# Kernel optimization log

Hardware: AMD Instinct MI355X
Metric: run time of the kernel (lower is better)

## Reference

```python
import jax, jax.numpy as jnp
import numpy as np

DIM = 512
HEADS = 8
DIM_HEAD = 64
INNER = HEADS * DIM_HEAD
CHUNK = 32
EPS = 1e-5


def _peg_conv(x, w, b):
    # x: (B, N, C); depthwise conv1d k=3 pad=1 applied on chunks of 32
    B, N, C = x.shape
    ns = -(-N // CHUNK)
    xp = jnp.pad(x, ((0, 0), (0, ns * CHUNK - N), (0, 0)))
    xp = xp.reshape(B * ns, CHUNK, C).transpose(0, 2, 1)  # (B*ns, C, 32)
    y = jax.lax.conv_general_dilated(
        xp, w, window_strides=(1,), padding=((1, 1),),
        dimension_numbers=("NCH", "OIH", "NCH"), feature_group_count=C)
    y = y + b[None, :, None]
    y = y.transpose(0, 2, 1).reshape(B, ns * CHUNK, C)[:, :N, :]
    return y


def _peg1d(x, w, b):
    p1 = _peg_conv(x, w, b)
    sx = jnp.roll(x, CHUNK // 2, axis=1)
    p2 = jnp.roll(_peg_conv(sx, w, b), -(CHUNK // 2), axis=1)
    return x + p1 + p2


def setup_inputs() -> dict:
    key = jax.random.key(0)
    ks = jax.random.split(key, 8)
    B, N, M = 2, 4096, 1024
    x = jax.random.normal(ks[0], (B, N, DIM), dtype=jnp.float32)
    mem = jax.random.normal(ks[1], (B, M, DIM), dtype=jnp.float32)
    w_qkv = jax.random.normal(ks[2], (DIM, 3 * INNER), dtype=jnp.float32) * 0.02
    w_out = jax.random.normal(ks[3], (INNER, DIM), dtype=jnp.float32) * 0.02
    b_out = jnp.zeros((DIM,), dtype=jnp.float32)
    ln_g = jnp.ones((DIM,), dtype=jnp.float32)
    ln_b = jnp.zeros((DIM,), dtype=jnp.float32)
    pk_w = jax.random.normal(ks[4], (DIM, 1, 3), dtype=jnp.float32) * 0.1
    pk_b = jnp.zeros((DIM,), dtype=jnp.float32)
    pv_w = jax.random.normal(ks[5], (DIM, 1, 3), dtype=jnp.float32) * 0.1
    pv_b = jnp.zeros((DIM,), dtype=jnp.float32)
    return {"x": x, "mem": mem, "ln_g": ln_g, "ln_b": ln_b,
            "w_qkv": w_qkv, "w_out": w_out, "b_out": b_out,
            "pk_w": pk_w, "pk_b": pk_b, "pv_w": pv_w, "pv_b": pv_b}


def reference(x, mem, ln_g, ln_b, w_qkv, w_out, b_out, pk_w, pk_b, pv_w, pv_b):
    B, N, _ = x.shape
    # LayerNorm
    mu = jnp.mean(x, axis=-1, keepdims=True)
    var = jnp.mean(jnp.square(x - mu), axis=-1, keepdims=True)
    xn = (x - mu) * jax.lax.rsqrt(var + EPS) * ln_g + ln_b
    qkv = xn @ w_qkv  # (B, N, 3*INNER)
    q, k, v = jnp.split(qkv, 3, axis=-1)
    # memory concat
    k = jnp.concatenate((k, mem), axis=1)
    v = jnp.concatenate((v, mem), axis=1)
    # PEG1D positional conv on k,v (excluding cls token at position 0)
    k = jnp.concatenate((k[:, :1, :], _peg1d(k[:, 1:, :], pk_w, pk_b)), axis=1)
    v = jnp.concatenate((v[:, :1, :], _peg1d(v[:, 1:, :], pv_w, pv_b)), axis=1)
    # split heads: b n (h d) -> b h n d
    Nk = k.shape[1]
    qh = q.reshape(B, N, HEADS, DIM_HEAD).transpose(0, 2, 1, 3)
    kh = k.reshape(B, Nk, HEADS, DIM_HEAD).transpose(0, 2, 1, 3)
    vh = v.reshape(B, Nk, HEADS, DIM_HEAD).transpose(0, 2, 1, 3)
    scale = DIM_HEAD ** -0.5
    dots = jnp.einsum("bhnd,bhmd->bhnm", qh, kh) * scale
    attn = jax.nn.softmax(dots, axis=-1)
    out = jnp.einsum("bhnm,bhmd->bhnd", attn, vh)
    out = out.transpose(0, 2, 1, 3).reshape(B, N, INNER)
    return out @ w_out + b_out
```

## Files before the change

kernel.cpp:

```cpp
#include <hip/hip_runtime.h>
#include <hip/hip_bf16.h>

typedef short short8 __attribute__((ext_vector_type(8)));
typedef __bf16 bf16x8 __attribute__((ext_vector_type(8)));
typedef float f32x4 __attribute__((ext_vector_type(4)));
typedef float f32x8 __attribute__((ext_vector_type(8)));
typedef float f32x16 __attribute__((ext_vector_type(16)));
typedef unsigned int uint4v __attribute__((ext_vector_type(4)));

#define SEQ_N 4096
#define NKEYS 5120
#define PEG_L 5119
#define NSPLIT 2
#define KEYS_PER_SPLIT 2560
#define NT_SPLIT 40

__device__ __forceinline__ float b2f(unsigned short s){
  union{unsigned u; float f;} v; v.u = ((unsigned)s)<<16; return v.f;
}
__device__ __forceinline__ unsigned short f2b(float f){
  unsigned u = __builtin_bit_cast(unsigned, f);
  u += 0x7fffu + ((u>>16)&1u);
  return (unsigned short)(u>>16);
}
__device__ __forceinline__ unsigned cvtpk(float lo, float hi){
  unsigned r;
  asm("v_cvt_pk_bf16_f32 %0, %1, %2" : "=v"(r) : "v"(lo), "v"(hi));
  return r;
}

__global__ void k_transpose_w(const float* __restrict__ src, unsigned short* __restrict__ dst,
                              int K, int Ncols){
  __shared__ float t[32][33];
  int tx = threadIdx.x, ty = threadIdx.y;
  int bx = blockIdx.x, by = blockIdx.y;
  #pragma unroll
  for (int i=0;i<4;i++){
    int r = by*32 + ty + 8*i, c = bx*32 + tx;
    t[ty+8*i][tx] = src[(size_t)r*Ncols + c];
  }
  __syncthreads();
  #pragma unroll
  for (int i=0;i<4;i++){
    int r = bx*32 + ty + 8*i, c = by*32 + tx;
    dst[(size_t)r*K + c] = f2b(t[tx][ty+8*i]);
  }
}

__global__ __launch_bounds__(256) void k_layernorm(const float* __restrict__ x,
    const float* __restrict__ g, const float* __restrict__ bb,
    unsigned short* __restrict__ xn){
  int w = threadIdx.x >> 6, l = threadIdx.x & 63;
  int row = blockIdx.x*4 + w;
  const float* xr = x + (size_t)row*512 + l*8;
  f32x4 a = *(const f32x4*)xr;
  f32x4 c4 = *(const f32x4*)(xr+4);
  float s = a[0]+a[1]+a[2]+a[3]+c4[0]+c4[1]+c4[2]+c4[3];
  #pragma unroll
  for (int d=1; d<64; d<<=1) s += __shfl_xor(s, d);
  float mu = s * (1.0f/512.0f);
  float vs = 0.f;
  #pragma unroll
  for (int i=0;i<4;i++){ float d0=a[i]-mu; vs += d0*d0; }
  #pragma unroll
  for (int i=0;i<4;i++){ float d0=c4[i]-mu; vs += d0*d0; }
  #pragma unroll
  for (int d=1; d<64; d<<=1) vs += __shfl_xor(vs, d);
  float rstd = rsqrtf(vs*(1.0f/512.0f) + 1e-5f);
  const float* gp = g + l*8;
  const float* bp = bb + l*8;
  unsigned short o[8];
  #pragma unroll
  for (int i=0;i<8;i++){
    float xi = (i<4)? a[i] : c4[i-4];
    o[i] = f2b((xi-mu)*rstd*gp[i] + bp[i]);
  }
  *(short8*)(xn + (size_t)row*512 + l*8) = *(short8*)o;
}

__global__ void k_memcat(const float* __restrict__ mem,
                         unsigned short* __restrict__ kf, unsigned short* __restrict__ vf){
  size_t e0 = ((size_t)blockIdx.x*256 + threadIdx.x)*8;
  f32x4 a = *(const f32x4*)(mem+e0);
  f32x4 c4 = *(const f32x4*)(mem+e0+4);
  unsigned short o[8];
  #pragma unroll
  for (int i=0;i<8;i++) o[i] = f2b((i<4)? a[i] : c4[i-4]);
  int c = (int)(e0 & 511);
  size_t row = e0 >> 9;
  size_t b = row >> 10, r = row & 1023;
  size_t dst = ((b*NKEYS) + 4096 + r)*512 + c;
  *(short8*)(kf+dst) = *(short8*)o;
  *(short8*)(vf+dst) = *(short8*)o;
}

template<int EPI>
__global__ __launch_bounds__(256) void k_gemm(const unsigned short* __restrict__ A,
    const unsigned short* __restrict__ BT, const float* __restrict__ bias,
    unsigned short* __restrict__ qb, unsigned short* __restrict__ kf,
    unsigned short* __restrict__ vf, float* __restrict__ outf){
  __shared__ unsigned short Al[64][72];
  __shared__ unsigned short Bl[64][72];
  const int tid = threadIdx.x;
  const int w = tid>>6, l = tid&63, m = l&15, hh = l>>4;
  const int m0 = blockIdx.x*64, n0 = blockIdx.y*64;
  const int srow = tid>>2, scg = tid&3;
  f32x4 acc[4];
  #pragma unroll
  for (int nt=0; nt<4; ++nt) acc[nt] = f32x4{0.f,0.f,0.f,0.f};
  const unsigned short* Ap = A + (size_t)(m0+srow)*512 + scg*8;
  const unsigned short* Bp = BT + (size_t)(n0+srow)*512 + scg*8;
  for (int kt=0; kt<8; ++kt){
    short8 a0 = *(const short8*)(Ap + kt*64);
    short8 a1 = *(const short8*)(Ap + kt*64 + 32);
    short8 b0 = *(const short8*)(Bp + kt*64);
    short8 b1 = *(const short8*)(Bp + kt*64 + 32);
    __syncthreads();
    *(short8*)&Al[srow][scg*8]      = a0;
    *(short8*)&Al[srow][32+scg*8]   = a1;
    *(short8*)&Bl[srow][scg*8]      = b0;
    *(short8*)&Bl[srow][32+scg*8]   = b1;
    __syncthreads();
    #pragma unroll
    for (int ks=0; ks<2; ++ks){
      bf16x8 af = *(const bf16x8*)&Al[w*16+m][ks*32 + hh*8];
      #pragma unroll
      for (int nt=0; nt<4; ++nt){
        bf16x8 bfv = *(const bf16x8*)&Bl[nt*16+m][ks*32 + hh*8];
        acc[nt] = __builtin_amdgcn_mfma_f32_16x16x32_bf16(af, bfv, acc[nt], 0,0,0);
      }
    }
  }
  #pragma unroll
  for (int nt=0; nt<4; ++nt){
    #pragma unroll
    for (int j=0; j<4; ++j){
      int grow = m0 + w*16 + 4*hh + j;
      int gcol = n0 + nt*16 + m;
      float v = acc[nt][j];
      if (EPI==0){
        int b = grow >> 12, n = grow & 4095;
        if (gcol < 512)       qb[(size_t)grow*512 + gcol] = f2b(v);
        else if (gcol < 1024) kf[((size_t)b*NKEYS + n)*512 + (gcol-512)]  = f2b(v);
        else                  vf[((size_t)b*NKEYS + n)*512 + (gcol-1024)] = f2b(v);
      } else {
        outf[(size_t)grow*512 + gcol] = v + bias[gcol];
      }
    }
  }
}

__global__ __launch_bounds__(256) void k_peg(const unsigned short* __restrict__ in,
    const float* __restrict__ w3, const float* __restrict__ bias,
    unsigned short* __restrict__ out){
  int idx = blockIdx.x*256 + threadIdx.x;
  int cg = idx & 63;
  int i  = (idx >> 6) % NKEYS;
  int b  = (idx >> 6) / NKEYS;
  int c0 = cg*8;
  const unsigned short* base = in + (size_t)b*NKEYS*512 + c0;
  unsigned short* op = out + ((size_t)b*NKEYS + i)*512 + c0;
  if (i == 0){ *(short8*)op = *(const short8*)base; return; }
  int j = i - 1;
  float wv0[8], wv1[8], wv2[8], bv[8], acc[8];
  #pragma unroll
  for (int k2=0;k2<8;k2++){
    wv0[k2] = w3[(c0+k2)*3 + 0];
    wv1[k2] = w3[(c0+k2)*3 + 1];
    wv2[k2] = w3[(c0+k2)*3 + 2];
    bv[k2]  = bias[c0+k2];
  }
  short8 xc = *(const short8*)(base + (size_t)i*512);
  #pragma unroll
  for (int k2=0;k2<8;k2++)
    acc[k2] = b2f((unsigned short)xc[k2]) * (1.0f + 2.0f*wv1[k2]) + 2.0f*bv[k2];
  int r = j & 31;
  int jj = j + 16; if (jj >= PEG_L) jj -= PEG_L;
  int r2 = jj & 31;
  if (r > 0){
    short8 xl = *(const short8*)(base + (size_t)j*512);
    #pragma unroll
    for (int k2=0;k2<8;k2++) acc[k2] += wv0[k2]*b2f((unsigned short)xl[k2]);
  }
  if (r < 31 && j+1 < PEG_L){
    short8 xr = *(const short8*)(base + (size_t)(j+2)*512);
    #pragma unroll
    for (int k2=0;k2<8;k2++) acc[k2] += wv2[k2]*b2f((unsigned short)xr[k2]);
  }
  if (r2 > 0){
    int p = jj - 17; if (p < 0) p += PEG_L;
    short8 xl = *(const short8*)(base + (size_t)(p+1)*512);
    #pragma unroll
    for (int k2=0;k2<8;k2++) acc[k2] += wv0[k2]*b2f((unsigned short)xl[k2]);
  }
  if (r2 < 31 && jj+1 < PEG_L){
    int p = jj - 15; if (p < 0) p += PEG_L;
    short8 xr = *(const short8*)(base + (size_t)(p+1)*512);
    #pragma unroll
    for (int k2=0;k2<8;k2++) acc[k2] += wv2[k2]*b2f((unsigned short)xr[k2]);
  }
  unsigned short o[8];
  #pragma unroll
  for (int k2=0;k2<8;k2++) o[k2] = f2b(acc[k2]);
  *(short8*)op = *(short8*)o;
}

__global__ __launch_bounds__(256) void k_vtrans(const unsigned short* __restrict__ vp,
                                                unsigned short* __restrict__ vpT){
  __shared__ unsigned short t[64][72];
  const int bh = blockIdx.y, b = bh>>3, h = bh&7;
  const int k0 = blockIdx.x*64;
  const int tid = threadIdx.x;
  #pragma unroll
  for (int it=0; it<2; ++it){
    int idx = tid + it*256;
    int key = idx>>3, dg = idx&7;
    short8 v = *(const short8*)(vp + ((size_t)b*NKEYS + k0+key)*512 + h*64 + dg*8);
    #pragma unroll
    for (int jj=0;jj<8;++jj) t[dg*8+jj][key] = (unsigned short)v[jj];
  }
  __syncthreads();
  #pragma unroll
  for (int it=0; it<2; ++it){
    int idx = tid + it*256;
    int d = idx>>3, kg = idx&7;
    short8 v = *(const short8*)&t[d][kg*8];
    *(short8*)(vpT + ((size_t)bh*64 + d)*NKEYS + k0 + kg*8) = v;
  }
}

__global__ __launch_bounds__(256, 4) void k_attn(
    const unsigned short* __restrict__ qb,
    const unsigned short* __restrict__ kp,
    const unsigned short* __restrict__ vpT,
    unsigned short* __restrict__ oP,
    float* __restrict__ ml){
  __shared__ unsigned short Kl[2][64][72];
  __shared__ unsigned short Vl[2][64][72];
  const int tid = threadIdx.x;
  const int w = tid >> 6, lid = tid & 63;
  const int lq = lid & 31, hi = lid >> 5;
  const int bh = blockIdx.y, b = bh >> 3, h = bh & 7;
  const int sp = blockIdx.z;
  const int q = blockIdx.x*128 + w*32 + lq;

  bf16x8 qreg[4];
  {
    const unsigned short* qr = qb + (size_t)(b*SEQ_N + q)*512 + h*64 + hi*8;
    #pragma unroll
    for (int dt=0; dt<4; ++dt) qreg[dt] = *(const bf16x8*)(qr + dt*16);
  }

  f32x16 o0 = {}, o1 = {};
  float mraw = -3.0e38f, lsum = 0.f;

  const int srow = tid >> 2, sg = tid & 3;
  const unsigned short* kst = kp + (size_t)b*NKEYS*512 + h*64
                              + (size_t)(sp*KEYS_PER_SPLIT)*512 + (size_t)srow*512 + sg*8;
  const unsigned short* vst = vpT + (size_t)bh*64*NKEYS + (size_t)srow*NKEYS
                              + sp*KEYS_PER_SPLIT + sg*8;

  {
    short8 a0 = *(const short8*)(kst);
    short8 a1 = *(const short8*)(kst + 32);
    short8 v0 = *(const short8*)(vst);
    short8 v1 = *(const short8*)(vst + 32);
    *(short8*)&Kl[0][srow][sg*8]    = a0;
    *(short8*)&Kl[0][srow][32+sg*8] = a1;
    *(short8*)&Vl[0][srow][sg*8]    = v0;
    *(short8*)&Vl[0][srow][32+sg*8] = v1;
  }
  __syncthreads();

  const float c2 = 0.18033688011f;
  int cur = 0;
  for (int kt=0; kt<NT_SPLIT; ++kt){
    short8 a0, a1, v0s, v1s;
    const bool pf = (kt+1) < NT_SPLIT;
    if (pf){
      const unsigned short* kn = kst + (size_t)(kt+1)*64*512;
      const unsigned short* vn = vst + (size_t)(kt+1)*64;
      a0  = *(const short8*)(kn);
      a1  = *(const short8*)(kn + 32);
      v0s = *(const short8*)(vn);
      v1s = *(const short8*)(vn + 32);
    }

    f32x16 s0 = {}, s1 = {};
    #pragma unroll
    for (int dt=0; dt<4; ++dt){
      bf16x8 kf0 = *(const bf16x8*)&Kl[cur][lq][dt*16 + hi*8];
      s0 = __builtin_amdgcn_mfma_f32_32x32x16_bf16(kf0, qreg[dt], s0, 0,0,0);
    }
    #pragma unroll
    for (int dt=0; dt<4; ++dt){
      bf16x8 kf1 = *(const bf16x8*)&Kl[cur][32+lq][dt*16 + hi*8];
      s1 = __builtin_amdgcn_mfma_f32_32x32x16_bf16(kf1, qreg[dt], s1, 0,0,0);
    }

    f32x8 sa0 = __builtin_shufflevector(s0, s0, 0,1,2,3,4,5,6,7);
    f32x8 sb0 = __builtin_shufflevector(s0, s0, 8,9,10,11,12,13,14,15);
    f32x8 sa1 = __builtin_shufflevector(s1, s1, 0,1,2,3,4,5,6,7);
    f32x8 sb1 = __builtin_shufflevector(s1, s1, 8,9,10,11,12,13,14,15);
    f32x8 mx8 = __builtin_elementwise_max(__builtin_elementwise_max(sa0, sb0),
                                          __builtin_elementwise_max(sa1, sb1));
    float pm = fmaxf(fmaxf(fmaxf(mx8[0],mx8[1]), fmaxf(mx8[2],mx8[3])),
                     fmaxf(fmaxf(mx8[4],mx8[5]), fmaxf(mx8[6],mx8[7])));

    if (!__all(pm <= mraw + 64.0f)){
      float pg = fmaxf(pm, __shfl_xor(pm, 32, 64));
      float mnew = fmaxf(mraw, pg);
      float al = exp2f((mraw - mnew)*c2);
      #pragma unroll
      for (int i=0;i<16;++i){ o0[i]*=al; o1[i]*=al; }
      lsum *= al;
      mraw = mnew;
    }
    const float nmc = -(mraw * c2);
    #pragma unroll
    for (int i=0;i<16;++i){
      s0[i] = exp2f(fmaf(s0[i], c2, nmc));
      s1[i] = exp2f(fmaf(s1[i], c2, nmc));
    }
    {
      f32x8 pa0 = __builtin_shufflevector(s0, s0, 0,1,2,3,4,5,6,7);
      f32x8 pb0 = __builtin_shufflevector(s0, s0, 8,9,10,11,12,13,14,15);
      f32x8 pa1 = __builtin_shufflevector(s1, s1, 0,1,2,3,4,5,6,7);
      f32x8 pb1 = __builtin_shufflevector(s1, s1, 8,9,10,11,12,13,14,15);
      f32x8 u = (pa0 + pb0) + (pa1 + pb1);
      f32x4 u4 = f32x4{u[0],u[1],u[2],u[3]} + f32x4{u[4],u[5],u[6],u[7]};
      lsum += (u4[0]+u4[1]) + (u4[2]+u4[3]);
    }

    #pragma unroll
    for (int sl=0; sl<4; ++sl){
      const f32x16& sv = (sl < 2) ? s0 : s1;
      const int rb = (sl & 1)*8;
      unsigned w0 = cvtpk(sv[rb+0], sv[rb+1]);
      unsigned w1 = cvtpk(sv[rb+2], sv[rb+3]);
      unsigned w2 = cvtpk(sv[rb+4], sv[rb+5]);
      unsigned w3 = cvtpk(sv[rb+6], sv[rb+7]);
      unsigned u0 = hi ? w0 : w2;
      unsigned u1 = hi ? w1 : w3;
      unsigned su0 = __shfl_xor(u0, 32, 64);
      unsigned su1 = __shfl_xor(u1, 32, 64);
      unsigned e0 = hi ? su0 : w0;
      unsigned e1 = hi ? su1 : w1;
      unsigned e2 = hi ? w2 : su0;
      unsigned e3 = hi ? w3 : su1;
      uint4v wv = {e0, e1, e2, e3};
      bf16x8 pb = __builtin_bit_cast(bf16x8, wv);
      bf16x8 vf0 = *(const bf16x8*)&Vl[cur][lq][sl*16 + hi*8];
      o0 = __builtin_amdgcn_mfma_f32_32x32x16_bf16(vf0, pb, o0, 0,0,0);
      bf16x8 vf1 = *(const bf16x8*)&Vl[cur][32+lq][sl*16 + hi*8];
      o1 = __builtin_amdgcn_mfma_f32_32x32x16_bf16(vf1, pb, o1, 0,0,0);
    }

    if (pf){
      *(short8*)&Kl[cur^1][srow][sg*8]    = a0;
      *(short8*)&Kl[cur^1][srow][32+sg*8] = a1;
      *(short8*)&Vl[cur^1][srow][sg*8]    = v0s;
      *(short8*)&Vl[cur^1][srow][32+sg*8] = v1s;
    }
    __syncthreads();
    cur ^= 1;
  }

  const float lt = lsum + __shfl_xor(lsum, 32, 64);
  const float inv = 1.0f / lt;
  unsigned short* op = oP + (((size_t)(sp*16 + bh)*SEQ_N + q)*64);
  #pragma unroll
  for (int r=0; r<16; r+=2){
    const int dloc = (r&3) + 8*(r>>2) + 4*hi;
    *(unsigned*)(op + dloc)      = cvtpk(o0[r]*inv, o0[r+1]*inv);
    *(unsigned*)(op + 32 + dloc) = cvtpk(o1[r]*inv, o1[r+1]*inv);
  }
  float* mlp = ml + ((size_t)(sp*16 + bh)*SEQ_N + q)*2;
  mlp[0] = mraw;
  mlp[1] = lt;
}

__global__ __launch_bounds__(256) void k_combine(const unsigned short* __restrict__ oP,
    const float* __restrict__ ml, unsigned short* __restrict__ attnb){
  const float c2 = 0.18033688011f;
  int idx = blockIdx.x*256 + threadIdx.x;
  int dg = idx & 7;
  int qbh = idx >> 3;
  int q = qbh & 4095;
  int bh = qbh >> 12;
  int b = bh >> 3, h = bh & 7;
  size_t i0 = ((size_t)bh*SEQ_N + q);
  size_t i1 = ((size_t)(16 + bh)*SEQ_N + q);
  short8 a = *(const short8*)(oP + i0*64 + dg*8);
  short8 c = *(const short8*)(oP + i1*64 + dg*8);
  float m0 = ml[i0*2], l0 = ml[i0*2+1];
  float m1 = ml[i1*2], l1 = ml[i1*2+1];
  float ms = fmaxf(m0, m1);
  float w0 = l0 * exp2f((m0 - ms)*c2);
  float w1 = l1 * exp2f((m1 - ms)*c2);
  float inv = 1.0f / (w0 + w1);
  float a0 = w0*inv, a1 = w1*inv;
  unsigned short o[8];
  #pragma unroll
  for (int k2=0;k2<8;k2++)
    o[k2] = f2b(a0*b2f((unsigned short)a[k2]) + a1*b2f((unsigned short)c[k2]));
  *(short8*)(attnb + ((size_t)(b*SEQ_N + q)*512) + h*64 + dg*8) = *(short8*)o;
}

extern "C" void kernel_launch(void* const* d_in, const int* in_sizes, int n_in,
                              void* d_out, int out_size, void* d_ws, size_t ws_size,
                              hipStream_t stream){
  const float* x     = (const float*)d_in[0];
  const float* mem   = (const float*)d_in[1];
  const float* ln_g  = (const float*)d_in[2];
  const float* ln_b  = (const float*)d_in[3];
  const float* w_qkv = (const float*)d_in[4];
  const float* w_out = (const float*)d_in[5];
  const float* b_out = (const float*)d_in[6];
  const float* pk_w  = (const float*)d_in[7];
  const float* pk_b  = (const float*)d_in[8];
  const float* pv_w  = (const float*)d_in[9];
  const float* pv_b  = (const float*)d_in[10];
  float* outp = (float*)d_out;

  char* ws = (char*)d_ws;
  size_t off = 0;
  auto alloc = [&](size_t bytes)->void*{
    void* p = ws + off; off += (bytes + 255) & ~(size_t)255; return p;
  };
  unsigned short* wqkvT = (unsigned short*)alloc((size_t)1536*512*2);
  unsigned short* woutT = (unsigned short*)alloc((size_t)512*512*2);
  unsigned short* xn    = (unsigned short*)alloc((size_t)8192*512*2);
  unsigned short* q_b   = (unsigned short*)alloc((size_t)8192*512*2);
  unsigned short* kf    = (unsigned short*)alloc((size_t)2*NKEYS*512*2);
  unsigned short* vf    = (unsigned short*)alloc((size_t)2*NKEYS*512*2);
  unsigned short* kpg   = (unsigned short*)alloc((size_t)2*NKEYS*512*2);
  unsigned short* vpg   = (unsigned short*)alloc((size_t)2*NKEYS*512*2);
  unsigned short* vpT   = (unsigned short*)alloc((size_t)2*NKEYS*512*2);
  unsigned short* attnb = (unsigned short*)alloc((size_t)8192*512*2);

  unsigned short* oP = kf;
  float* ml = (float*)((char*)kf + (size_t)NSPLIT*16*SEQ_N*64*2);

  k_transpose_w<<<dim3(48,16), dim3(32,8), 0, stream>>>(w_qkv, wqkvT, 512, 1536);
  k_transpose_w<<<dim3(16,16), dim3(32,8), 0, stream>>>(w_out, woutT, 512, 512);
  k_layernorm<<<2048, 256, 0, stream>>>(x, ln_g, ln_b, xn);
  k_memcat<<<512, 256, 0, stream>>>(mem, kf, vf);
  k_gemm<0><<<dim3(128,24), 256, 0, stream>>>(xn, wqkvT, nullptr, q_b, kf, vf, nullptr);
  k_peg<<<2560, 256, 0, stream>>>(kf, pk_w, pk_b, kpg);
  k_peg<<<2560, 256, 0, stream>>>(vf, pv_w, pv_b, vpg);
  k_vtrans<<<dim3(80,16), 256, 0, stream>>>(vpg, vpT);
  k_attn<<<dim3(32,16,NSPLIT), 256, 0, stream>>>(q_b, kpg, vpT, oP, ml);
  k_combine<<<2048, 256, 0, stream>>>(oP, ml, attnb);
  k_gemm<1><<<dim3(128,8), 256, 0, stream>>>(attnb, woutT, b_out, nullptr, nullptr, nullptr, outp);
}
```

Before: 312.7 us.

## Split key tile into two 32-key halves with per-half online softmax and MFMA priority

The flash-attention inner loop now handles each 64-key tile as two 32-key halves. Each half computes QK^T, updates the running max and rescales, exponentiates and runs its PV MFMAs before the next half starts. This halves the live score registers and lets softmax work of one half interleave with MFMA work. The MFMA sections are also wrapped in s_setprio so waves issuing matrix ops get priority. The cost is twice as many max checks and possible rescales per tile.

```diff
diff --git a/kernel.cpp b/kernel.cpp
--- a/kernel.cpp
+++ b/kernel.cpp
@@ -274,39 +274,14 @@
 
   const float c2 = 0.18033688011f;
   int cur = 0;
-  for (int kt=0; kt<NT_SPLIT; ++kt){
-    short8 a0, a1, v0s, v1s;
-    const bool pf = (kt+1) < NT_SPLIT;
-    if (pf){
-      const unsigned short* kn = kst + (size_t)(kt+1)*64*512;
-      const unsigned short* vn = vst + (size_t)(kt+1)*64;
-      a0  = *(const short8*)(kn);
-      a1  = *(const short8*)(kn + 32);
-      v0s = *(const short8*)(vn);
-      v1s = *(const short8*)(vn + 32);
-    }
-
-    f32x16 s0 = {}, s1 = {};
-    #pragma unroll
-    for (int dt=0; dt<4; ++dt){
-      bf16x8 kf0 = *(const bf16x8*)&Kl[cur][lq][dt*16 + hi*8];
-      s0 = __builtin_amdgcn_mfma_f32_32x32x16_bf16(kf0, qreg[dt], s0, 0,0,0);
-    }
-    #pragma unroll
-    for (int dt=0; dt<4; ++dt){
-      bf16x8 kf1 = *(const bf16x8*)&Kl[cur][32+lq][dt*16 + hi*8];
-      s1 = __builtin_amdgcn_mfma_f32_32x32x16_bf16(kf1, qreg[dt], s1, 0,0,0);
-    }
-
-    f32x8 sa0 = __builtin_shufflevector(s0, s0, 0,1,2,3,4,5,6,7);
-    f32x8 sb0 = __builtin_shufflevector(s0, s0, 8,9,10,11,12,13,14,15);
-    f32x8 sa1 = __builtin_shufflevector(s1, s1, 0,1,2,3,4,5,6,7);
-    f32x8 sb1 = __builtin_shufflevector(s1, s1, 8,9,10,11,12,13,14,15);
-    f32x8 mx8 = __builtin_elementwise_max(__builtin_elementwise_max(sa0, sb0),
-                                          __builtin_elementwise_max(sa1, sb1));
-    float pm = fmaxf(fmaxf(fmaxf(mx8[0],mx8[1]), fmaxf(mx8[2],mx8[3])),
-                     fmaxf(fmaxf(mx8[4],mx8[5]), fmaxf(mx8[6],mx8[7])));
-
+
+  auto process32 = [&](f32x16 s, const int slb){
+    f32x8 sl8 = __builtin_shufflevector(s, s, 0,1,2,3,4,5,6,7);
+    f32x8 sh8 = __builtin_shufflevector(s, s, 8,9,10,11,12,13,14,15);
+    f32x8 m8 = __builtin_elementwise_max(sl8, sh8);
+    f32x4 m4 = __builtin_elementwise_max(f32x4{m8[0],m8[1],m8[2],m8[3]},
+                                         f32x4{m8[4],m8[5],m8[6],m8[7]});
+    float pm = fmaxf(fmaxf(m4[0],m4[1]), fmaxf(m4[2],m4[3]));
     if (!__all(pm <= mraw + 64.0f)){
       float pg = fmaxf(pm, __shfl_xor(pm, 32, 64));
       float mnew = fmaxf(mraw, pg);
@@ -318,28 +293,22 @@
     }
     const float nmc = -(mraw * c2);
     #pragma unroll
-    for (int i=0;i<16;++i){
-      s0[i] = exp2f(fmaf(s0[i], c2, nmc));
-      s1[i] = exp2f(fmaf(s1[i], c2, nmc));
-    }
+    for (int i=0;i<16;++i) s[i] = exp2f(fmaf(s[i], c2, nmc));
     {
-      f32x8 pa0 = __builtin_shufflevector(s0, s0, 0,1,2,3,4,5,6,7);
-      f32x8 pb0 = __builtin_shufflevector(s0, s0, 8,9,10,11,12,13,14,15);
-      f32x8 pa1 = __builtin_shufflevector(s1, s1, 0,1,2,3,4,5,6,7);
-      f32x8 pb1 = __builtin_shufflevector(s1, s1, 8,9,10,11,12,13,14,15);
-      f32x8 u = (pa0 + pb0) + (pa1 + pb1);
+      f32x8 pa = __builtin_shufflevector(s, s, 0,1,2,3,4,5,6,7);
+      f32x8 pb8 = __builtin_shufflevector(s, s, 8,9,10,11,12,13,14,15);
+      f32x8 u = pa + pb8;
       f32x4 u4 = f32x4{u[0],u[1],u[2],u[3]} + f32x4{u[4],u[5],u[6],u[7]};
       lsum += (u4[0]+u4[1]) + (u4[2]+u4[3]);
     }
-
-    #pragma unroll
-    for (int sl=0; sl<4; ++sl){
-      const f32x16& sv = (sl < 2) ? s0 : s1;
-      const int rb = (sl & 1)*8;
-      unsigned w0 = cvtpk(sv[rb+0], sv[rb+1]);
-      unsigned w1 = cvtpk(sv[rb+2], sv[rb+3]);
-      unsigned w2 = cvtpk(sv[rb+4], sv[rb+5]);
-      unsigned w3 = cvtpk(sv[rb+6], sv[rb+7]);
+    #pragma unroll
+    for (int k2=0; k2<2; ++k2){
+      const int sl = slb + k2;
+      const int rb = k2*8;
+      unsigned w0 = cvtpk(s[rb+0], s[rb+1]);
+      unsigned w1 = cvtpk(s[rb+2], s[rb+3]);
+      unsigned w2 = cvtpk(s[rb+4], s[rb+5]);
+      unsigned w3 = cvtpk(s[rb+6], s[rb+7]);
       unsigned u0 = hi ? w0 : w2;
       unsigned u1 = hi ? w1 : w3;
       unsigned su0 = __shfl_xor(u0, 32, 64);
@@ -351,9 +320,47 @@
       uint4v wv = {e0, e1, e2, e3};
       bf16x8 pb = __builtin_bit_cast(bf16x8, wv);
       bf16x8 vf0 = *(const bf16x8*)&Vl[cur][lq][sl*16 + hi*8];
+      bf16x8 vf1 = *(const bf16x8*)&Vl[cur][32+lq][sl*16 + hi*8];
+      __builtin_amdgcn_s_setprio(1);
       o0 = __builtin_amdgcn_mfma_f32_32x32x16_bf16(vf0, pb, o0, 0,0,0);
-      bf16x8 vf1 = *(const bf16x8*)&Vl[cur][32+lq][sl*16 + hi*8];
       o1 = __builtin_amdgcn_mfma_f32_32x32x16_bf16(vf1, pb, o1, 0,0,0);
+      __builtin_amdgcn_s_setprio(0);
+    }
+  };
+
+  for (int kt=0; kt<NT_SPLIT; ++kt){
+    short8 a0, a1, v0s, v1s;
+    const bool pf = (kt+1) < NT_SPLIT;
+    if (pf){
+      const unsigned short* kn = kst + (size_t)(kt+1)*64*512;
+      const unsigned short* vn = vst + (size_t)(kt+1)*64;
+      a0  = *(const short8*)(kn);
+      a1  = *(const short8*)(kn + 32);
+      v0s = *(const short8*)(vn);
+      v1s = *(const short8*)(vn + 32);
+    }
+
+    {
+      f32x16 s = {};
+      __builtin_amdgcn_s_setprio(1);
+      #pragma unroll
+      for (int dt=0; dt<4; ++dt){
+        bf16x8 kf0 = *(const bf16x8*)&Kl[cur][lq][dt*16 + hi*8];
+        s = __builtin_amdgcn_mfma_f32_32x32x16_bf16(kf0, qreg[dt], s, 0,0,0);
+      }
+      __builtin_amdgcn_s_setprio(0);
+      process32(s, 0);
+    }
+    {
+      f32x16 s = {};
+      __builtin_amdgcn_s_setprio(1);
+      #pragma unroll
+      for (int dt=0; dt<4; ++dt){
+        bf16x8 kf1 = *(const bf16x8*)&Kl[cur][32+lq][dt*16 + hi*8];
+        s = __builtin_amdgcn_mfma_f32_32x32x16_bf16(kf1, qreg[dt], s, 0,0,0);
+      }
+      __builtin_amdgcn_s_setprio(0);
+      process32(s, 2);
     }
 
     if (pf){
```

Result: no change. 311.1 us (-0.5%).

## Enlarge GEMM tiles to 128x128 and use fast exp2/rcp intrinsics in attention

Applied to the files above, without the earlier changes.

The GEMM kernel moves from 64x64 to 128x128 tiles, so each wave computes a 32x128 sub-tile with 16 MFMA accumulators. This increases reuse of operands staged in LDS and cuts global traffic per flop, at the cost of fewer blocks and higher register and LDS use. The attention and combine kernels switch exp2f and the final division to hardware approximate intrinsics. The attention kernel also keeps the row sum as an 8-wide vector until the end, taking the horizontal reduction out of the inner loop.

```diff
diff --git a/kernel.cpp b/kernel.cpp
--- a/kernel.cpp
+++ b/kernel.cpp
@@ -95,56 +95,71 @@
 }
 
 template<int EPI>
-__global__ __launch_bounds__(256) void k_gemm(const unsigned short* __restrict__ A,
+__global__ __launch_bounds__(256) void k_gemm2(const unsigned short* __restrict__ A,
     const unsigned short* __restrict__ BT, const float* __restrict__ bias,
     unsigned short* __restrict__ qb, unsigned short* __restrict__ kf,
     unsigned short* __restrict__ vf, float* __restrict__ outf){
-  __shared__ unsigned short Al[64][72];
-  __shared__ unsigned short Bl[64][72];
+  __shared__ unsigned short Al[128][72];
+  __shared__ unsigned short Bl[128][72];
   const int tid = threadIdx.x;
   const int w = tid>>6, l = tid&63, m = l&15, hh = l>>4;
-  const int m0 = blockIdx.x*64, n0 = blockIdx.y*64;
-  const int srow = tid>>2, scg = tid&3;
-  f32x4 acc[4];
-  #pragma unroll
-  for (int nt=0; nt<4; ++nt) acc[nt] = f32x4{0.f,0.f,0.f,0.f};
-  const unsigned short* Ap = A + (size_t)(m0+srow)*512 + scg*8;
-  const unsigned short* Bp = BT + (size_t)(n0+srow)*512 + scg*8;
+  const int m0 = blockIdx.x*128, n0 = blockIdx.y*128;
+  f32x4 acc[2][8];
+  #pragma unroll
+  for (int mt=0; mt<2; ++mt)
+    #pragma unroll
+    for (int nt=0; nt<8; ++nt) acc[mt][nt] = f32x4{0.f,0.f,0.f,0.f};
+
   for (int kt=0; kt<8; ++kt){
-    short8 a0 = *(const short8*)(Ap + kt*64);
-    short8 a1 = *(const short8*)(Ap + kt*64 + 32);
-    short8 b0 = *(const short8*)(Bp + kt*64);
-    short8 b1 = *(const short8*)(Bp + kt*64 + 32);
+    short8 av[4], bv[4];
+    #pragma unroll
+    for (int i=0;i<4;++i){
+      int c = tid + i*256;
+      int row = c >> 3, c8 = (c & 7)*8;
+      av[i] = *(const short8*)(A  + (size_t)(m0+row)*512 + kt*64 + c8);
+      bv[i] = *(const short8*)(BT + (size_t)(n0+row)*512 + kt*64 + c8);
+    }
     __syncthreads();
-    *(short8*)&Al[srow][scg*8]      = a0;
-    *(short8*)&Al[srow][32+scg*8]   = a1;
-    *(short8*)&Bl[srow][scg*8]      = b0;
-    *(short8*)&Bl[srow][32+scg*8]   = b1;
+    #pragma unroll
+    for (int i=0;i<4;++i){
+      int c = tid + i*256;
+      int row = c >> 3, c8 = (c & 7)*8;
+      *(short8*)&Al[row][c8] = av[i];
+      *(short8*)&Bl[row][c8] = bv[i];
+    }
     __syncthreads();
     #pragma unroll
     for (int ks=0; ks<2; ++ks){
-      bf16x8 af = *(const bf16x8*)&Al[w*16+m][ks*32 + hh*8];
+      bf16x8 af[2];
       #pragma unroll
-      for (int nt=0; nt<4; ++nt){
+      for (int mt=0; mt<2; ++mt)
+        af[mt] = *(const bf16x8*)&Al[w*32 + mt*16 + m][ks*32 + hh*8];
+      #pragma unroll
+      for (int nt=0; nt<8; ++nt){
         bf16x8 bfv = *(const bf16x8*)&Bl[nt*16+m][ks*32 + hh*8];
-        acc[nt] = __builtin_amdgcn_mfma_f32_16x16x32_bf16(af, bfv, acc[nt], 0,0,0);
+        #pragma unroll
+        for (int mt=0; mt<2; ++mt)
+          acc[mt][nt] = __builtin_amdgcn_mfma_f32_16x16x32_bf16(af[mt], bfv, acc[mt][nt], 0,0,0);
       }
     }
   }
   #pragma unroll
-  for (int nt=0; nt<4; ++nt){
-    #pragma unroll
-    for (int j=0; j<4; ++j){
-      int grow = m0 + w*16 + 4*hh + j;
-      int gcol = n0 + nt*16 + m;
-      float v = acc[nt][j];
-      if (EPI==0){
-        int b = grow >> 12, n = grow & 4095;
-        if (gcol < 512)       qb[(size_t)grow*512 + gcol] = f2b(v);
-        else if (gcol < 1024) kf[((size_t)b*NKEYS + n)*512 + (gcol-512)]  = f2b(v);
-        else                  vf[((size_t)b*NKEYS + n)*512 + (gcol-1024)] = f2b(v);
-      } else {
-        outf[(size_t)grow*512 + gcol] = v + bias[gcol];
+  for (int mt=0; mt<2; ++mt){
+    #pragma unroll
+    for (int nt=0; nt<8; ++nt){
+      #pragma unroll
+      for (int j=0; j<4; ++j){
+        int grow = m0 + w*32 + mt*16 + 4*hh + j;
+        int gcol = n0 + nt*16 + m;
+        float v = acc[mt][nt][j];
+        if (EPI==0){
+          int b = grow >> 12, n = grow & 4095;
+          if (gcol < 512)       qb[(size_t)grow*512 + gcol] = f2b(v);
+          else if (gcol < 1024) kf[((size_t)b*NKEYS + n)*512 + (gcol-512)]  = f2b(v);
+          else                  vf[((size_t)b*NKEYS + n)*512 + (gcol-1024)] = f2b(v);
+        } else {
+          outf[(size_t)grow*512 + gcol] = v + bias[gcol];
+        }
       }
     }
   }
@@ -252,7 +267,8 @@
   }
 
   f32x16 o0 = {}, o1 = {};
-  float mraw = -3.0e38f, lsum = 0.f;
+  f32x8 lsum8 = {};
+  float mraw = -3.0e38f;
 
   const int srow = tid >> 2, sg = tid & 3;
   const unsigned short* kst = kp + (size_t)b*NKEYS*512 + h*64
@@ -310,26 +326,25 @@
     if (!__all(pm <= mraw + 64.0f)){
       float pg = fmaxf(pm, __shfl_xor(pm, 32, 64));
       float mnew = fmaxf(mraw, pg);
-      float al = exp2f((mraw - mnew)*c2);
+      float al = __builtin_amdgcn_exp2f((mraw - mnew)*c2);
       #pragma unroll
       for (int i=0;i<16;++i){ o0[i]*=al; o1[i]*=al; }
-      lsum *= al;
+      #pragma unroll
+      for (int i=0;i<8;++i) lsum8[i] *= al;
       mraw = mnew;
     }
     const float nmc = -(mraw * c2);
     #pragma unroll
     for (int i=0;i<16;++i){
-      s0[i] = exp2f(fmaf(s0[i], c2, nmc));
-      s1[i] = exp2f(fmaf(s1[i], c2, nmc));
+      s0[i] = __builtin_amdgcn_exp2f(fmaf(s0[i], c2, nmc));
+      s1[i] = __builtin_amdgcn_exp2f(fmaf(s1[i], c2, nmc));
     }
     {
       f32x8 pa0 = __builtin_shufflevector(s0, s0, 0,1,2,3,4,5,6,7);
       f32x8 pb0 = __builtin_shufflevector(s0, s0, 8,9,10,11,12,13,14,15);
       f32x8 pa1 = __builtin_shufflevector(s1, s1, 0,1,2,3,4,5,6,7);
       f32x8 pb1 = __builtin_shufflevector(s1, s1, 8,9,10,11,12,13,14,15);
-      f32x8 u = (pa0 + pb0) + (pa1 + pb1);
-      f32x4 u4 = f32x4{u[0],u[1],u[2],u[3]} + f32x4{u[4],u[5],u[6],u[7]};
-      lsum += (u4[0]+u4[1]) + (u4[2]+u4[3]);
+      lsum8 += (pa0 + pb0) + (pa1 + pb1);
     }
 
     #pragma unroll
@@ -366,8 +381,10 @@
     cur ^= 1;
   }
 
+  f32x4 l4 = f32x4{lsum8[0],lsum8[1],lsum8[2],lsum8[3]} + f32x4{lsum8[4],lsum8[5],lsum8[6],lsum8[7]};
+  float lsum = (l4[0]+l4[1]) + (l4[2]+l4[3]);
   const float lt = lsum + __shfl_xor(lsum, 32, 64);
-  const float inv = 1.0f / lt;
+  const float inv = __builtin_amdgcn_rcpf(lt);
   unsigned short* op = oP + (((size_t)(sp*16 + bh)*SEQ_N + q)*64);
   #pragma unroll
   for (int r=0; r<16; r+=2){
@@ -396,8 +413,8 @@
   float m0 = ml[i0*2], l0 = ml[i0*2+1];
   float m1 = ml[i1*2], l1 = ml[i1*2+1];
   float ms = fmaxf(m0, m1);
-  float w0 = l0 * exp2f((m0 - ms)*c2);
-  float w1 = l1 * exp2f((m1 - ms)*c2);
+  float w0 = l0 * __builtin_amdgcn_exp2f((m0 - ms)*c2);
+  float w1 = l1 * __builtin_amdgcn_exp2f((m1 - ms)*c2);
   float inv = 1.0f / (w0 + w1);
   float a0 = w0*inv, a1 = w1*inv;
   unsigned short o[8];
@@ -446,11 +463,11 @@
   k_transpose_w<<<dim3(16,16), dim3(32,8), 0, stream>>>(w_out, woutT, 512, 512);
   k_layernorm<<<2048, 256, 0, stream>>>(x, ln_g, ln_b, xn);
   k_memcat<<<512, 256, 0, stream>>>(mem, kf, vf);
-  k_gemm<0><<<dim3(128,24), 256, 0, stream>>>(xn, wqkvT, nullptr, q_b, kf, vf, nullptr);
+  k_gemm2<0><<<dim3(64,12), 256, 0, stream>>>(xn, wqkvT, nullptr, q_b, kf, vf, nullptr);
   k_peg<<<2560, 256, 0, stream>>>(kf, pk_w, pk_b, kpg);
   k_peg<<<2560, 256, 0, stream>>>(vf, pv_w, pv_b, vpg);
   k_vtrans<<<dim3(80,16), 256, 0, stream>>>(vpg, vpT);
   k_attn<<<dim3(32,16,NSPLIT), 256, 0, stream>>>(q_b, kpg, vpT, oP, ml);
   k_combine<<<2048, 256, 0, stream>>>(oP, ml, attnb);
-  k_gemm<1><<<dim3(128,8), 256, 0, stream>>>(attnb, woutT, b_out, nullptr, nullptr, nullptr, outp);
-}
+  k_gemm2<1><<<dim3(64,4), 256, 0, stream>>>(attnb, woutT, b_out, nullptr, nullptr, nullptr, outp);
+}
```

New measurement: 282.3 us. -9.7%, faster.
